# Optimization experiments

Hardware: AMD Instinct MI355X
Metric: run time of the kernel (lower is better)

The kernel has to match this reference:

```python
import jax, jax.numpy as jnp
import numpy as np

N, C, H, W = 16, 256, 48, 96
S = 64   # num_s = 2*num_state_mid; also num_n = mids*mids = 64 (must match)
EPS = 1e-5


def setup_inputs() -> dict:
    key = jax.random.key(0)
    ks = jax.random.split(key, 11)
    sc = 0.05
    return {
        "x": jax.random.normal(ks[0], (N, C, H, W), jnp.float32),
        "edge": jax.random.normal(ks[1], (N, 2, H, W), jnp.float32),
        # conv_state: Conv2d(C, S, 1) with bias
        "Ws": jax.random.normal(ks[2], (S, C), jnp.float32) * sc,
        "bs": jax.random.normal(ks[3], (S,), jnp.float32) * sc,
        # conv_proj: Conv2d(C, S, 1) with bias
        "Wp": jax.random.normal(ks[4], (S, C), jnp.float32) * sc,
        "bp": jax.random.normal(ks[5], (S,), jnp.float32) * sc,
        # GCN conv1: Conv1d(num_n, num_n, 1, bias=False)
        "W1": jax.random.normal(ks[6], (S, S), jnp.float32) * sc,
        # GCN conv2: Conv1d(S, S, 1, bias=False)
        "W2": jax.random.normal(ks[7], (S, S), jnp.float32) * sc,
        # conv_extend: Conv2d(S, C, 1, bias=False)
        "We": jax.random.normal(ks[8], (C, S), jnp.float32) * sc,
        # BatchNorm2d(C) affine params (training-mode batch stats used in forward)
        "gamma": jnp.ones((C,), jnp.float32),
        "beta": jnp.zeros((C,), jnp.float32),
    }


def reference(x, edge, Ws, bs, Wp, bp, W1, W2, We, gamma, beta):
    n, c, h, w = x.shape
    s = Ws.shape[0]
    # edge softmax over channels, take class-1 probability map  -> (n,1,h,w)
    edge_g = jax.nn.softmax(edge, axis=1)[:, 1:2]

    # 1x1 convs as channel matmuls
    xs = jnp.einsum('oc,nchw->nohw', Ws, x) + bs[None, :, None, None]
    xs = xs.reshape(n, s, h * w)                        # (n,S,HW)
    xp = jnp.einsum('oc,nchw->nohw', Wp, x) + bp[None, :, None, None]
    # x_proj_region + x_proj_edge == xp * (1 + edge_gate)
    comb = (xp * (1.0 + edge_g)).reshape(n, s, h * w)
    comb = jax.nn.softmax(comb, axis=-1)                # softmax over spatial

    # project to graph space: (n,S,HW) @ (n,HW,S) -> (n,S,S)
    xn = jnp.einsum('nsk,ntk->nst', xs, comb)

    # GCN: conv1 over node dim (last axis mixes via W1), subtract, conv2 over state dim, relu
    hh = jnp.einsum('ij,nsj->nsi', W1, xn) - xn
    hh = jax.nn.relu(jnp.einsum('ij,njk->nik', W2, hh))

    # back-project: (n,S,S) @ (n,S,HW) -> (n,S,HW) -> (n,S,H,W)
    xr = jnp.einsum('nst,ntk->nsk', hh, comb).reshape(n, s, h, w)

    # conv_extend (no bias) then BatchNorm2d in training mode (biased batch var)
    ext = jnp.einsum('os,nshw->nohw', We, xr)
    mean = ext.mean(axis=(0, 2, 3), keepdims=True)
    var = ext.var(axis=(0, 2, 3), keepdims=True)
    bn = gamma[None, :, None, None] * (ext - mean) * jax.lax.rsqrt(var + EPS) \
         + beta[None, :, None, None]
    return x + bn
```

## Files before the change

kernel.cpp:

```cpp
#include <hip/hip_runtime.h>

#define HW 4608
#define NB 16
#define CC 256
#define SS 64
#define EPS 1e-5f
#define NSPLIT 24

typedef __attribute__((ext_vector_type(8))) short short8;
typedef __attribute__((ext_vector_type(4))) float f32x4;

__device__ __forceinline__ ushort f2bf(float f) {
    uint u = __float_as_uint(f);
    return (ushort)((u + 0x7FFFu + ((u >> 16) & 1u)) >> 16);
}
__device__ __forceinline__ float bf2f(ushort h) {
    return __uint_as_float(((uint)h) << 16);
}

__global__ __launch_bounds__(256) void k_wf(const float* __restrict__ Ws,
                                            const float* __restrict__ Wp,
                                            ushort* __restrict__ Wf) {
    int idx = blockIdx.x * 256 + threadIdx.x;
    int j = idx & 7, r = (idx >> 3) & 127, kq = (idx >> 10) & 3, cs = idx >> 12;
    int c = cs * 32 + kq * 8 + j;
    float v = (r < 64) ? Ws[r * CC + c] : Wp[(r - 64) * CC + c];
    Wf[idx] = f2bf(v);
}

__global__ __launch_bounds__(256) void k_proj(const float* __restrict__ x,
                                              const ushort* __restrict__ Wf,
                                              const float* __restrict__ bs,
                                              const float* __restrict__ bp,
                                              const float* __restrict__ edge,
                                              ushort* __restrict__ xsb,
                                              ushort* __restrict__ Eb,
                                              float* __restrict__ rsum) {
    __shared__ __align__(16) ushort Bl[4 * 128 * 8];
    int n = blockIdx.y, k0 = blockIdx.x * 128;
    int tid = threadIdx.x, lane = tid & 63, w = tid >> 6;
    int wr = w >> 1, wn = w & 1;
    int q = lane >> 4, li = lane & 15;
    int sn = tid & 127, kq0 = (tid >> 7) * 2;
    f32x4 acc[4][4] = {};
    for (int cs = 0; cs < 8; cs++) {
#pragma unroll
        for (int kk = 0; kk < 2; kk++) {
            int kq = kq0 + kk;
            union { ushort u[8]; uint4 v; } tmp;
#pragma unroll
            for (int j = 0; j < 8; j++) {
                float vv = x[((size_t)n * CC + cs * 32 + kq * 8 + j) * HW + k0 + sn];
                tmp.u[j] = f2bf(vv);
            }
            *(uint4*)&Bl[(kq * 128 + sn) * 8] = tmp.v;
        }
        __syncthreads();
        short8 af[4], bfr[4];
#pragma unroll
        for (int m = 0; m < 4; m++) {
            int r = wr * 64 + m * 16 + li;
            uint4 t = *(const uint4*)&Wf[((cs * 4 + q) * 128 + r) * 8];
            af[m] = *(short8*)&t;
        }
#pragma unroll
        for (int nn = 0; nn < 4; nn++) {
            int nl = wn * 64 + nn * 16 + li;
            uint4 t = *(const uint4*)&Bl[(q * 128 + nl) * 8];
            bfr[nn] = *(short8*)&t;
        }
#pragma unroll
        for (int m = 0; m < 4; m++)
#pragma unroll
            for (int nn = 0; nn < 4; nn++)
                acc[m][nn] = __builtin_amdgcn_mfma_f32_16x16x32_bf16(af[m], bfr[nn], acc[m][nn], 0, 0, 0);
        __syncthreads();
    }
    if (wr == 0) {
#pragma unroll
        for (int m = 0; m < 4; m++) {
#pragma unroll
            for (int rr = 0; rr < 4; rr++) {
                int s = m * 16 + q * 4 + rr;
                float bv = bs[s];
#pragma unroll
                for (int nn = 0; nn < 4; nn++) {
                    int col = k0 + wn * 64 + nn * 16 + li;
                    xsb[((size_t)n * SS + s) * HW + col] = f2bf(acc[m][nn][rr] + bv);
                }
            }
        }
    } else {
        float ga[4];
#pragma unroll
        for (int nn = 0; nn < 4; nn++) {
            int col = k0 + wn * 64 + nn * 16 + li;
            float e0 = edge[((size_t)n * 2 + 0) * HW + col];
            float e1 = edge[((size_t)n * 2 + 1) * HW + col];
            ga[nn] = 1.f + 1.f / (1.f + __expf(e0 - e1));
        }
        float rp[4][4];
#pragma unroll
        for (int m = 0; m < 4; m++) {
#pragma unroll
            for (int rr = 0; rr < 4; rr++) {
                int s = m * 16 + q * 4 + rr;
                float bv = bp[s];
                float sum = 0.f;
#pragma unroll
                for (int nn = 0; nn < 4; nn++) {
                    int col = k0 + wn * 64 + nn * 16 + li;
                    float e = __expf((acc[m][nn][rr] + bv) * ga[nn]);
                    sum += e;
                    Eb[((size_t)n * SS + s) * HW + col] = f2bf(e);
                }
                rp[m][rr] = sum;
            }
        }
#pragma unroll
        for (int b = 1; b < 16; b <<= 1)
#pragma unroll
            for (int m = 0; m < 4; m++)
#pragma unroll
                for (int rr = 0; rr < 4; rr++)
                    rp[m][rr] += __shfl_xor(rp[m][rr], b, 64);
        if (li == 0) {
#pragma unroll
            for (int m = 0; m < 4; m++)
#pragma unroll
                for (int rr = 0; rr < 4; rr++)
                    atomicAdd(&rsum[n * SS + m * 16 + q * 4 + rr], rp[m][rr]);
        }
    }
}

__global__ __launch_bounds__(256) void k_graph(const ushort* __restrict__ xsb,
                                               const ushort* __restrict__ Eb,
                                               float* __restrict__ Up,
                                               float* __restrict__ Pp) {
    int n = blockIdx.y, sp = blockIdx.x;
    int kbase = sp * (HW / NSPLIT);
    int tid = threadIdx.x, lane = tid & 63, w = tid >> 6;
    int q = lane >> 4, li = lane & 15;
    bool isP = w >= 2;
    int half = w & 1;
    const ushort* Arow = isP ? Eb : xsb;
    f32x4 acc[2][4] = {};
    for (int ks = 0; ks < (HW / NSPLIT) / 32; ks++) {
        int kb = kbase + ks * 32 + q * 8;
        short8 af[2], bfr[4];
#pragma unroll
        for (int mt = 0; mt < 2; mt++) {
            int s = half * 32 + mt * 16 + li;
            uint4 t = *(const uint4*)&Arow[((size_t)n * SS + s) * HW + kb];
            af[mt] = *(short8*)&t;
        }
#pragma unroll
        for (int nt = 0; nt < 4; nt++) {
            int tt = nt * 16 + li;
            uint4 t = *(const uint4*)&Eb[((size_t)n * SS + tt) * HW + kb];
            bfr[nt] = *(short8*)&t;
        }
#pragma unroll
        for (int mt = 0; mt < 2; mt++)
#pragma unroll
            for (int nt = 0; nt < 4; nt++)
                acc[mt][nt] = __builtin_amdgcn_mfma_f32_16x16x32_bf16(af[mt], bfr[nt], acc[mt][nt], 0, 0, 0);
    }
    float* dst = (isP ? Pp : Up) + ((size_t)sp * NB + n) * 4096;
#pragma unroll
    for (int mt = 0; mt < 2; mt++)
#pragma unroll
        for (int nt = 0; nt < 4; nt++)
#pragma unroll
            for (int rr = 0; rr < 4; rr++) {
                int row = half * 32 + mt * 16 + q * 4 + rr;
                int col = nt * 16 + li;
                dst[row * 64 + col] = acc[mt][nt][rr];
            }
}

__global__ __launch_bounds__(256) void k_red(const float* __restrict__ Up,
                                             const float* __restrict__ Pp,
                                             float* __restrict__ U,
                                             float* __restrict__ P) {
    int idx = blockIdx.x * 256 + threadIdx.x;
    const float* src = (idx < 16384) ? Up : Pp;
    float* dst = (idx < 16384) ? U : P;
    int o = (idx & 16383) * 4;
    f32x4 s = {};
    for (int sp = 0; sp < NSPLIT; sp++) {
        f32x4 v = *(const f32x4*)&src[(size_t)sp * 65536 + o];
        s += v;
    }
    *(f32x4*)&dst[o] = s;
}

__global__ __launch_bounds__(256) void k_gcn(const float* __restrict__ U,
                                             const float* __restrict__ rsum,
                                             const float* __restrict__ W1,
                                             const float* __restrict__ W2,
                                             const float* __restrict__ We,
                                             float* __restrict__ M,
                                             ushort* __restrict__ Mf) {
    __shared__ __align__(16) float A[64 * 68];
    __shared__ __align__(16) float B[64 * 68];
    __shared__ __align__(16) float Cb[64 * 68];
    __shared__ float rs[64];
    int n = blockIdx.x;
    int cc = blockIdx.y;
    int tid = threadIdx.x;
    int t0 = tid >> 4, t1 = tid & 15;
    if (tid < 64) rs[tid] = 1.0f / rsum[n * SS + tid];
    __syncthreads();
#pragma unroll
    for (int i = 0; i < 16; i++) {
        int idx = tid + i * 256;
        int r = idx >> 6, cth = idx & 63;
        A[cth * 68 + r] = U[n * 4096 + idx] * rs[cth];
        B[cth * 68 + r] = W1[idx];
    }
    __syncthreads();
    {
        float acc[4][4] = {};
        for (int j = 0; j < 64; j++) {
            float4 a4 = *(const float4*)&A[j * 68 + t0 * 4];
            float4 b4 = *(const float4*)&B[j * 68 + t1 * 4];
            float a[4] = {a4.x, a4.y, a4.z, a4.w};
            float b[4] = {b4.x, b4.y, b4.z, b4.w};
#pragma unroll
            for (int p = 0; p < 4; p++)
#pragma unroll
                for (int qq = 0; qq < 4; qq++) acc[p][qq] += a[p] * b[qq];
        }
#pragma unroll
        for (int p = 0; p < 4; p++)
#pragma unroll
            for (int qq = 0; qq < 4; qq++) {
                acc[p][qq] -= A[(t1 * 4 + qq) * 68 + (t0 * 4 + p)];
                Cb[(t0 * 4 + p) * 68 + t1 * 4 + qq] = acc[p][qq];
            }
    }
    __syncthreads();
#pragma unroll
    for (int i = 0; i < 16; i++) {
        int idx = tid + i * 256;
        int r = idx >> 6, cth = idx & 63;
        B[cth * 68 + r] = W2[idx];
    }
    __syncthreads();
    {
        float acc[4][4] = {};
        for (int j = 0; j < 64; j++) {
            float4 a4 = *(const float4*)&B[j * 68 + t0 * 4];
            float4 b4 = *(const float4*)&Cb[j * 68 + t1 * 4];
            float a[4] = {a4.x, a4.y, a4.z, a4.w};
            float b[4] = {b4.x, b4.y, b4.z, b4.w};
#pragma unroll
            for (int p = 0; p < 4; p++)
#pragma unroll
                for (int qq = 0; qq < 4; qq++) acc[p][qq] += a[p] * b[qq];
        }
        __syncthreads();
#pragma unroll
        for (int p = 0; p < 4; p++)
#pragma unroll
            for (int qq = 0; qq < 4; qq++)
                A[(t0 * 4 + p) * 68 + t1 * 4 + qq] = fmaxf(acc[p][qq], 0.f);
    }
    __syncthreads();
#pragma unroll
    for (int i = 0; i < 16; i++) {
        int idx = tid + i * 256;
        int c = idx >> 6, j = idx & 63;
        B[j * 68 + c] = We[(cc * 64 + c) * 64 + j];
    }
    __syncthreads();
    {
        float acc[4][4] = {};
        for (int j = 0; j < 64; j++) {
            float4 a4 = *(const float4*)&B[j * 68 + t0 * 4];
            float4 b4 = *(const float4*)&A[j * 68 + t1 * 4];
            float a[4] = {a4.x, a4.y, a4.z, a4.w};
            float b[4] = {b4.x, b4.y, b4.z, b4.w};
#pragma unroll
            for (int p = 0; p < 4; p++)
#pragma unroll
                for (int qq = 0; qq < 4; qq++) acc[p][qq] += a[p] * b[qq];
        }
#pragma unroll
        for (int p = 0; p < 4; p++) {
            int c = cc * 64 + t0 * 4 + p;
            float v[4];
#pragma unroll
            for (int qq = 0; qq < 4; qq++) v[qq] = acc[p][qq] * rs[t1 * 4 + qq];
            float4 st = {v[0], v[1], v[2], v[3]};
            *(float4*)&M[((size_t)n * CC + c) * 64 + t1 * 4] = st;
#pragma unroll
            for (int qq = 0; qq < 4; qq++) {
                int t = t1 * 4 + qq;
                Mf[(size_t)n * 16384 + ((t >> 3) * 256 + c) * 8 + (t & 7)] = f2bf(v[qq]);
            }
        }
    }
}

__global__ __launch_bounds__(256) void k_stats(const float* __restrict__ M,
                                               const float* __restrict__ P,
                                               const float* __restrict__ rsum,
                                               const float* __restrict__ gamma,
                                               const float* __restrict__ beta,
                                               float* __restrict__ sc,
                                               float* __restrict__ bi) {
    __shared__ float ms[NB][64];
    __shared__ float red[256];
    int c = blockIdx.x;
    int tid = threadIdx.x;
    for (int i = tid; i < NB * 64; i += 256) {
        int n = i >> 6, s = i & 63;
        ms[n][s] = M[((size_t)n * CC + c) * 64 + s];
    }
    __syncthreads();
    float qa = 0.f;
    for (int n = 0; n < NB; n++) {
        const float* Pn = P + n * 4096;
#pragma unroll
        for (int p = 0; p < 16; p++) {
            int e = p * 256 + tid;
            qa += ms[n][e >> 6] * ms[n][e & 63] * Pn[e];
        }
    }
    float sa = 0.f;
    for (int i = tid; i < NB * 64; i += 256) {
        int n = i >> 6, s = i & 63;
        sa += ms[n][s] * rsum[n * SS + s];
    }
    red[tid] = qa;
    __syncthreads();
    for (int off = 128; off > 0; off >>= 1) {
        if (tid < off) red[tid] += red[tid + off];
        __syncthreads();
    }
    float qtot = red[0];
    __syncthreads();
    red[tid] = sa;
    __syncthreads();
    for (int off = 128; off > 0; off >>= 1) {
        if (tid < off) red[tid] += red[tid + off];
        __syncthreads();
    }
    if (tid == 0) {
        float stot = red[0];
        const float invM = 1.0f / ((float)NB * (float)HW);
        float mean = stot * invM;
        float var = qtot * invM - mean * mean;
        float s = gamma[c] * rsqrtf(var + EPS);
        sc[c] = s;
        bi[c] = beta[c] - s * mean;
    }
}

__global__ __launch_bounds__(256) void k_out(const float* __restrict__ x,
                                             const ushort* __restrict__ Mf,
                                             const ushort* __restrict__ Eb,
                                             const float* __restrict__ sc,
                                             const float* __restrict__ bi,
                                             float* __restrict__ out) {
    __shared__ __align__(16) ushort Bl[8 * 64 * 8];
    int n = blockIdx.y, k0 = blockIdx.x * 64;
    int tid = threadIdx.x, lane = tid & 63, w = tid >> 6;
    int q = lane >> 4, li = lane & 15;
    {
        int nl = tid & 63, pr = tid >> 6;
#pragma unroll
        for (int kk = 0; kk < 2; kk++) {
            int kq = pr * 2 + kk;
            union { ushort u[8]; uint4 v; } tmp;
#pragma unroll
            for (int j = 0; j < 8; j++)
                tmp.u[j] = Eb[((size_t)n * SS + kq * 8 + j) * HW + k0 + nl];
            *(uint4*)&Bl[(kq * 64 + nl) * 8] = tmp.v;
        }
    }
    __syncthreads();
    f32x4 acc[4][4] = {};
#pragma unroll
    for (int ks = 0; ks < 2; ks++) {
        short8 af[4], bfr[4];
#pragma unroll
        for (int mt = 0; mt < 4; mt++) {
            int c = w * 64 + mt * 16 + li;
            uint4 t = *(const uint4*)&Mf[(size_t)n * 16384 + ((ks * 4 + q) * 256 + c) * 8];
            af[mt] = *(short8*)&t;
        }
#pragma unroll
        for (int nt = 0; nt < 4; nt++) {
            int nl = nt * 16 + li;
            uint4 t = *(const uint4*)&Bl[((ks * 4 + q) * 64 + nl) * 8];
            bfr[nt] = *(short8*)&t;
        }
#pragma unroll
        for (int mt = 0; mt < 4; mt++)
#pragma unroll
            for (int nt = 0; nt < 4; nt++)
                acc[mt][nt] = __builtin_amdgcn_mfma_f32_16x16x32_bf16(af[mt], bfr[nt], acc[mt][nt], 0, 0, 0);
    }
#pragma unroll
    for (int mt = 0; mt < 4; mt++) {
#pragma unroll
        for (int rr = 0; rr < 4; rr++) {
            int c = w * 64 + mt * 16 + q * 4 + rr;
            float s_ = sc[c], bv = bi[c];
            size_t base = ((size_t)n * CC + c) * HW + k0;
#pragma unroll
            for (int nt = 0; nt < 4; nt++) {
                int col = nt * 16 + li;
                out[base + col] = x[base + col] + s_ * acc[mt][nt][rr] + bv;
            }
        }
    }
}

extern "C" void kernel_launch(void* const* d_in, const int* in_sizes, int n_in,
                              void* d_out, int out_size, void* d_ws, size_t ws_size,
                              hipStream_t stream) {
    const float* x = (const float*)d_in[0];
    const float* edge = (const float*)d_in[1];
    const float* Ws = (const float*)d_in[2];
    const float* bs = (const float*)d_in[3];
    const float* Wp = (const float*)d_in[4];
    const float* bp = (const float*)d_in[5];
    const float* W1 = (const float*)d_in[6];
    const float* W2 = (const float*)d_in[7];
    const float* We = (const float*)d_in[8];
    const float* gamma = (const float*)d_in[9];
    const float* beta = (const float*)d_in[10];
    float* out = (float*)d_out;

    char* base = (char*)d_ws;
    ushort* Wf  = (ushort*)base;                    base += 65536;
    ushort* xsb = (ushort*)base;                    base += 9437184;
    ushort* Eb  = (ushort*)base;                    base += 9437184;
    float*  Up  = (float*)base;                     base += (size_t)NSPLIT * NB * 4096 * 4;
    float*  Pp  = (float*)base;                     base += (size_t)NSPLIT * NB * 4096 * 4;
    float*  U   = (float*)base;                     base += 262144;
    float*  P   = (float*)base;                     base += 262144;
    float*  rsum= (float*)base;                     base += 4096;
    float*  M   = (float*)base;                     base += 1048576;
    ushort* Mf  = (ushort*)base;                    base += 524288;
    float*  sc  = (float*)base;                     base += 1024;
    float*  bi  = (float*)base;                     base += 1024;

    hipMemsetAsync(rsum, 0, 1024 * sizeof(float), stream);
    k_wf<<<128, 256, 0, stream>>>(Ws, Wp, Wf);
    k_proj<<<dim3(36, NB), 256, 0, stream>>>(x, Wf, bs, bp, edge, xsb, Eb, rsum);
    k_graph<<<dim3(NSPLIT, NB), 256, 0, stream>>>(xsb, Eb, Up, Pp);
    k_red<<<128, 256, 0, stream>>>(Up, Pp, U, P);
    k_gcn<<<dim3(NB, 4), 256, 0, stream>>>(U, rsum, W1, W2, We, M, Mf);
    k_stats<<<256, 256, 0, stream>>>(M, P, rsum, gamma, beta, sc, bi);
    k_out<<<dim3(72, NB), 256, 0, stream>>>(x, Mf, Eb, sc, bi, out);
}
```

Measured before the change: 233.0 us.

## Halve projection tile width and prefetch next x/W slices into registers

```diff
diff --git a/kernel.cpp b/kernel.cpp
--- a/kernel.cpp
+++ b/kernel.cpp
@@ -36,100 +36,104 @@
                                               ushort* __restrict__ xsb,
                                               ushort* __restrict__ Eb,
                                               float* __restrict__ rsum) {
-    __shared__ __align__(16) ushort Bl[4 * 128 * 8];
-    int n = blockIdx.y, k0 = blockIdx.x * 128;
+    __shared__ __align__(16) ushort Bl[4 * 64 * 8];
+    int n = blockIdx.y, k0 = blockIdx.x * 64;
     int tid = threadIdx.x, lane = tid & 63, w = tid >> 6;
-    int wr = w >> 1, wn = w & 1;
     int q = lane >> 4, li = lane & 15;
-    int sn = tid & 127, kq0 = (tid >> 7) * 2;
-    f32x4 acc[4][4] = {};
+    f32x4 acc[2][4] = {};
+    const float* xb = x + (size_t)n * CC * HW + k0 + lane;
+    float pf[8];
+    uint4 afn[2];
+#pragma unroll
+    for (int j = 0; j < 8; j++) pf[j] = xb[(size_t)(w * 8 + j) * HW];
+#pragma unroll
+    for (int mt = 0; mt < 2; mt++)
+        afn[mt] = *(const uint4*)&Wf[((0 * 4 + q) * 128 + w * 32 + mt * 16 + li) * 8];
+#pragma unroll 1
     for (int cs = 0; cs < 8; cs++) {
-#pragma unroll
-        for (int kk = 0; kk < 2; kk++) {
-            int kq = kq0 + kk;
-            union { ushort u[8]; uint4 v; } tmp;
-#pragma unroll
-            for (int j = 0; j < 8; j++) {
-                float vv = x[((size_t)n * CC + cs * 32 + kq * 8 + j) * HW + k0 + sn];
-                tmp.u[j] = f2bf(vv);
-            }
-            *(uint4*)&Bl[(kq * 128 + sn) * 8] = tmp.v;
-        }
+        union { ushort u[8]; uint4 v; } tmp;
+#pragma unroll
+        for (int j = 0; j < 8; j++) tmp.u[j] = f2bf(pf[j]);
+        short8 af[2];
+        af[0] = *(short8*)&afn[0];
+        af[1] = *(short8*)&afn[1];
+        *(uint4*)&Bl[(w * 64 + lane) * 8] = tmp.v;
         __syncthreads();
-        short8 af[4], bfr[4];
-#pragma unroll
-        for (int m = 0; m < 4; m++) {
-            int r = wr * 64 + m * 16 + li;
-            uint4 t = *(const uint4*)&Wf[((cs * 4 + q) * 128 + r) * 8];
-            af[m] = *(short8*)&t;
-        }
-#pragma unroll
-        for (int nn = 0; nn < 4; nn++) {
-            int nl = wn * 64 + nn * 16 + li;
-            uint4 t = *(const uint4*)&Bl[(q * 128 + nl) * 8];
-            bfr[nn] = *(short8*)&t;
-        }
-#pragma unroll
-        for (int m = 0; m < 4; m++)
-#pragma unroll
-            for (int nn = 0; nn < 4; nn++)
-                acc[m][nn] = __builtin_amdgcn_mfma_f32_16x16x32_bf16(af[m], bfr[nn], acc[m][nn], 0, 0, 0);
+        if (cs < 7) {
+#pragma unroll
+            for (int j = 0; j < 8; j++)
+                pf[j] = xb[(size_t)((cs + 1) * 32 + w * 8 + j) * HW];
+#pragma unroll
+            for (int mt = 0; mt < 2; mt++)
+                afn[mt] = *(const uint4*)&Wf[(((cs + 1) * 4 + q) * 128 + w * 32 + mt * 16 + li) * 8];
+        }
+        short8 bfr[4];
+#pragma unroll
+        for (int nt = 0; nt < 4; nt++) {
+            uint4 t = *(const uint4*)&Bl[(q * 64 + nt * 16 + li) * 8];
+            bfr[nt] = *(short8*)&t;
+        }
+#pragma unroll
+        for (int mt = 0; mt < 2; mt++)
+#pragma unroll
+            for (int nt = 0; nt < 4; nt++)
+                acc[mt][nt] = __builtin_amdgcn_mfma_f32_16x16x32_bf16(af[mt], bfr[nt], acc[mt][nt], 0, 0, 0);
         __syncthreads();
     }
-    if (wr == 0) {
-#pragma unroll
-        for (int m = 0; m < 4; m++) {
+    if (w < 2) {
+#pragma unroll
+        for (int mt = 0; mt < 2; mt++) {
 #pragma unroll
             for (int rr = 0; rr < 4; rr++) {
-                int s = m * 16 + q * 4 + rr;
+                int s = w * 32 + mt * 16 + q * 4 + rr;
                 float bv = bs[s];
 #pragma unroll
-                for (int nn = 0; nn < 4; nn++) {
-                    int col = k0 + wn * 64 + nn * 16 + li;
-                    xsb[((size_t)n * SS + s) * HW + col] = f2bf(acc[m][nn][rr] + bv);
+                for (int nt = 0; nt < 4; nt++) {
+                    int col = k0 + nt * 16 + li;
+                    xsb[((size_t)n * SS + s) * HW + col] = f2bf(acc[mt][nt][rr] + bv);
                 }
             }
         }
     } else {
         float ga[4];
 #pragma unroll
-        for (int nn = 0; nn < 4; nn++) {
-            int col = k0 + wn * 64 + nn * 16 + li;
+        for (int nt = 0; nt < 4; nt++) {
+            int col = k0 + nt * 16 + li;
             float e0 = edge[((size_t)n * 2 + 0) * HW + col];
             float e1 = edge[((size_t)n * 2 + 1) * HW + col];
-            ga[nn] = 1.f + 1.f / (1.f + __expf(e0 - e1));
-        }
-        float rp[4][4];
-#pragma unroll
-        for (int m = 0; m < 4; m++) {
+            ga[nt] = 1.f + 1.f / (1.f + __expf(e0 - e1));
+        }
+        float rp[2][4];
+#pragma unroll
+        for (int mt = 0; mt < 2; mt++) {
 #pragma unroll
             for (int rr = 0; rr < 4; rr++) {
-                int s = m * 16 + q * 4 + rr;
+                int s = (w - 2) * 32 + mt * 16 + q * 4 + rr;
                 float bv = bp[s];
                 float sum = 0.f;
 #pragma unroll
-                for (int nn = 0; nn < 4; nn++) {
-                    int col = k0 + wn * 64 + nn * 16 + li;
-                    float e = __expf((acc[m][nn][rr] + bv) * ga[nn]);
+                for (int nt = 0; nt < 4; nt++) {
+                    int col = k0 + nt * 16 + li;
+                    float e = __expf((acc[mt][nt][rr] + bv) * ga[nt]);
                     sum += e;
                     Eb[((size_t)n * SS + s) * HW + col] = f2bf(e);
                 }
-                rp[m][rr] = sum;
+                rp[mt][rr] = sum;
             }
         }
 #pragma unroll
         for (int b = 1; b < 16; b <<= 1)
 #pragma unroll
-            for (int m = 0; m < 4; m++)
+            for (int mt = 0; mt < 2; mt++)
 #pragma unroll
                 for (int rr = 0; rr < 4; rr++)
-                    rp[m][rr] += __shfl_xor(rp[m][rr], b, 64);
+                    rp[mt][rr] += __shfl_xor(rp[mt][rr], b, 64);
         if (li == 0) {
 #pragma unroll
-            for (int m = 0; m < 4; m++)
+            for (int mt = 0; mt < 2; mt++)
 #pragma unroll
                 for (int rr = 0; rr < 4; rr++)
-                    atomicAdd(&rsum[n * SS + m * 16 + q * 4 + rr], rp[m][rr]);
+                    atomicAdd(&rsum[n * SS + (w - 2) * 32 + mt * 16 + q * 4 + rr], rp[mt][rr]);
         }
     }
 }
@@ -453,7 +457,7 @@
 
     hipMemsetAsync(rsum, 0, 1024 * sizeof(float), stream);
     k_wf<<<128, 256, 0, stream>>>(Ws, Wp, Wf);
-    k_proj<<<dim3(36, NB), 256, 0, stream>>>(x, Wf, bs, bp, edge, xsb, Eb, rsum);
+    k_proj<<<dim3(72, NB), 256, 0, stream>>>(x, Wf, bs, bp, edge, xsb, Eb, rsum);
     k_graph<<<dim3(NSPLIT, NB), 256, 0, stream>>>(xsb, Eb, Up, Pp);
     k_red<<<128, 256, 0, stream>>>(Up, Pp, U, P);
     k_gcn<<<dim3(NB, 4), 256, 0, stream>>>(U, rsum, W1, W2, We, M, Mf);
```

Result: faster. 223.4 us (-4.1%).
